# Kernel tuning notes

Hardware: AMD Instinct MI355X
Metric: run time of the kernel (lower is better)

Reference implementation:

```python
import jax, jax.numpy as jnp
import numpy as np

B, H, W = 4, 112, 112
N = H * W              # 12544 tokens
NBHD = 48              # local neighborhood size
DIM = 256
OUT_DIM = 512
INNER = 4              # inner_ch of weight_net
TABLE = 4096           # pre_table rows
ALPHA = 4.0
DS_RATE = 0.25
STRIDE = 2
RESERVE = (H // 4) * (W // 4)  # 784 reserve tokens (pos % 4 == 0)
EPS = 1e-5


def _ln(x, g, b):
    m = x.mean(-1, keepdims=True)
    v = ((x - m) ** 2).mean(-1, keepdims=True)
    return (x - m) / jnp.sqrt(v + EPS) * g + b


def setup_inputs() -> dict:
    key = jax.random.key(0)
    ks = jax.random.split(key, 8)
    ii, jj = jnp.meshgrid(jnp.arange(H), jnp.arange(W), indexing='ij')
    pos = jnp.stack([ii, jj], -1).reshape(1, N, 2).astype(jnp.float32)
    pos = jnp.tile(pos, (B, 1, 1))                             # b x n x 2 integer grid
    feat = jax.random.normal(ks[0], (B, N, DIM), jnp.float32)
    member_idx = jax.random.randint(ks[1], (B, N, NBHD), 0, N)
    cluster_mask = (jax.random.uniform(ks[2], (B, N, NBHD)) > 0.1).astype(jnp.float32)
    learned_prob = jax.random.uniform(ks[3], (B, N, 1), dtype=jnp.float32)
    pe_idx = jax.random.randint(ks[4], (B, N, NBHD), 0, TABLE)
    pre_table = jax.random.normal(ks[5], (TABLE, 5), jnp.float32)
    w1 = jax.random.normal(ks[6], (5, INNER), jnp.float32) * 0.4
    b1 = jnp.zeros((INNER,), jnp.float32)
    ln1_g = jnp.ones((INNER,), jnp.float32)
    ln1_b = jnp.zeros((INNER,), jnp.float32)
    norm_g = jnp.ones((INNER * DIM,), jnp.float32)
    norm_b = jnp.zeros((INNER * DIM,), jnp.float32)
    lin_w = jax.random.normal(ks[7], (INNER * DIM, OUT_DIM), jnp.float32) * (1.0 / np.sqrt(INNER * DIM))
    lin_b = jnp.zeros((OUT_DIM,), jnp.float32)
    return dict(pos=pos, feat=feat, member_idx=member_idx, cluster_mask=cluster_mask,
                learned_prob=learned_prob, stride=STRIDE, pe_idx=pe_idx, reserve_num=RESERVE,
                pre_table=pre_table, w1=w1, b1=b1, ln1_g=ln1_g, ln1_b=ln1_b,
                norm_g=norm_g, norm_b=norm_b, lin_w=lin_w, lin_b=lin_b)


def reference(pos, feat, member_idx, cluster_mask, learned_prob, stride, pe_idx,
              reserve_num, pre_table, w1, b1, ln1_g, ln1_b, norm_g, norm_b, lin_w, lin_b):
    b, n, c = feat.shape
    keep_num = int(n * DS_RATE)
    pos_long = pos.astype(jnp.int32)
    # stride == 2 branch: tokens on the coarse grid get prob 1
    grid_prob = jnp.all(pos_long % stride == 0, axis=-1).astype(jnp.float32)      # b x n
    lp_s = jax.lax.stop_gradient(learned_prob).reshape(b, n) * ALPHA              # detached scores
    final_prob = grid_prob + lp_s
    reserve_mask = jnp.all(pos_long % (stride * 2) == 0, axis=-1).astype(jnp.float32)
    final_prob = final_prob + reserve_mask * (-100.0)
    sample_num = keep_num - reserve_num
    _, sample_idx = jax.lax.top_k(final_prob, sample_num)                         # b x sample_num
    # per-row nonzero of reserve_mask (exactly reserve_num hits per row)
    flat_nz = jnp.nonzero(reserve_mask.reshape(-1) > 0, size=b * reserve_num)[0]
    reserve_idx = (flat_nz % n).reshape(b, reserve_num).astype(sample_idx.dtype)
    idx = jnp.concatenate([sample_idx, reserve_idx], axis=1)                      # b x keep_num

    pos_k = jnp.take_along_axis(pos, idx[:, :, None], axis=1)                     # b x keep x 2
    nbhd = member_idx.shape[-1]
    mem_k = jnp.take_along_axis(member_idx, idx[:, :, None], axis=1)              # b x keep x nbhd
    pe_k = jnp.take_along_axis(pe_idx, idx[:, :, None], axis=1)
    cm_k = jnp.take_along_axis(cluster_mask, idx[:, :, None], axis=1)
    lp = jnp.take_along_axis(learned_prob, mem_k.reshape(b, -1, 1), axis=1)
    lp = lp.reshape(b, keep_num, nbhd, 1)

    # weight_net on the small PE table, then gather per-edge weights
    wt = jax.nn.gelu(_ln(pre_table @ w1 + b1, ln1_g, ln1_b), approximate=False)   # TABLE x INNER
    weights = wt[pe_k]                                                            # b x keep x nbhd x INNER
    weights = weights * (lp * cm_k[..., None])

    # CLUSTENWF: gather neighbor features and weighted-sum over the neighborhood
    gathered = jnp.take_along_axis(feat, mem_k.reshape(b, -1, 1), axis=1)
    gathered = gathered.reshape(b, keep_num, nbhd, c)                             # b x keep x nbhd x c
    out = jnp.einsum('bnkm,bnkc->bnmc', weights, gathered).reshape(b, keep_num, INNER * c)
    out = _ln(out, norm_g, norm_b)
    return pos_k, out @ lin_w + lin_b
```

## Files before the change

### kernel.cpp

```cpp
#include <hip/hip_runtime.h>

typedef unsigned short u16;
typedef unsigned int u32;
typedef unsigned long long u64;

#define NB 4
#define NTOK 12544
#define NBHD 48
#define DIM 256
#define OUTD 512
#define KEEPN 3136
#define SAMPLEN 2352
#define RESN 784
#define GW 112
#define POSN (NB * KEEPN * 2)
#define QTR (NTOK / 4)
#define NBKT 16384

#define BLKM 128
#define BLKN 256
#define BROW 40

#define FEATB_BYTES (25690112ull)
#define XWS_BYTES   (25690112ull)
#define LINT_BYTES  (1048576ull)
#define KEYS_BYTES  (401408ull)
#define PART_BYTES  (802816ull)
#define WS_NEED (FEATB_BYTES + XWS_BYTES + LINT_BYTES + KEYS_BYTES + PART_BYTES)

__device__ __forceinline__ float bf2f(u16 u) {
    union { u32 i; float f; } v; v.i = ((u32)u) << 16; return v.f;
}
__device__ __forceinline__ float asf(u32 u) {
    union { u32 i; float f; } v; v.i = u; return v.f;
}
__device__ __forceinline__ u16 f2bf(float f) {
    union { u32 i; float f; } v; v.f = f;
    return (u16)((v.i + 0x7FFFu + ((v.i >> 16) & 1u)) >> 16);
}

typedef __bf16 bf16x8 __attribute__((ext_vector_type(8)));
typedef float floatx4 __attribute__((ext_vector_type(4)));

__device__ __forceinline__ float make_f(float lp, int n) {
    int i = n / GW, j = n % GW;
    float f = lp * 4.0f;
    if (((i | j) & 1) == 0) f = 1.0f + f;
    if (((i | j) & 3) == 0) f = f + (-100.0f);
    return f;
}
__device__ __forceinline__ u64 f_to_key(float f, int n) {
    union { float f; u32 u; } v; v.f = f;
    u32 m = (v.u & 0x80000000u) ? ~v.u : (v.u | 0x80000000u);
    return (((u64)m) << 32) | (u64)(0xFFFFFFFFu - (u32)n);
}
__device__ __forceinline__ int f_to_bucket(float f) {
    int b = (int)floorf(f * 3276.8f);
    return b < 0 ? 0 : (b > NBKT - 1 ? NBKT - 1 : b);
}

__global__ __launch_bounds__(256) void feat_cvt_kernel(
    const float* __restrict__ feat, u16* __restrict__ featb) {
    int t = blockIdx.x * 256 + threadIdx.x;
    float4 v = ((const float4*)feat)[t];
    u64 w = (u64)f2bf(v.x) | ((u64)f2bf(v.y) << 16) |
            ((u64)f2bf(v.z) << 32) | ((u64)f2bf(v.w) << 48);
    ((u64*)featb)[t] = w;
}

__global__ __launch_bounds__(256) void linT_cvt_kernel(
    const float* __restrict__ lin_w, u16* __restrict__ linT) {
    __shared__ u16 T[64 * 65];
    int k0 = blockIdx.x * 64, n0 = blockIdx.y * 64;
    int t = threadIdx.x;
    int r = t >> 2, c4 = (t & 3) * 16;
#pragma unroll
    for (int i = 0; i < 4; ++i) {
        float4 v = *(const float4*)&lin_w[(size_t)(k0 + r) * OUTD + n0 + c4 + i * 4];
        T[(c4 + i * 4 + 0) * 65 + r] = f2bf(v.x);
        T[(c4 + i * 4 + 1) * 65 + r] = f2bf(v.y);
        T[(c4 + i * 4 + 2) * 65 + r] = f2bf(v.z);
        T[(c4 + i * 4 + 3) * 65 + r] = f2bf(v.w);
    }
    __syncthreads();
    int nl = t >> 2, kc = (t & 3) * 16;
    union { uint4 v[2]; u16 h[16]; } u;
#pragma unroll
    for (int i = 0; i < 16; ++i) u.h[i] = T[nl * 65 + kc + i];
    u16* dst = &linT[(size_t)(n0 + nl) * 1024 + k0 + kc];
    *(uint4*)(dst + 0) = u.v[0];
    *(uint4*)(dst + 8) = u.v[1];
}

__global__ __launch_bounds__(256) void zero_hist_kernel(u32* __restrict__ hist) {
    hist[blockIdx.x * 256 + threadIdx.x] = 0;
}

__global__ __launch_bounds__(256) void hist_kernel(
    const float* __restrict__ lprob, u32* __restrict__ hist) {
    int g = blockIdx.x * 256 + threadIdx.x;
    int b = g / NTOK, n = g % NTOK;
    int bkt = f_to_bucket(make_f(lprob[g], n));
    atomicAdd(&hist[b * NBKT + bkt], 1u);
}

__global__ __launch_bounds__(1024) void prefix_kernel(
    const u32* __restrict__ hist, u32* __restrict__ base, u32* __restrict__ cursor) {
    int b = blockIdx.x, t = threadIdx.x;
    const u32* h = hist + b * NBKT;
    u32 loc[16], own = 0;
#pragma unroll
    for (int i = 0; i < 16; ++i) { loc[i] = h[t * 16 + i]; own += loc[i]; }
    __shared__ u32 buf[2][1024];
    buf[0][t] = own;
    __syncthreads();
    int src = 0;
    for (int off = 1; off < 1024; off <<= 1) {
        u32 v = buf[src][t] + ((t + off < 1024) ? buf[src][t + off] : 0u);
        buf[src ^ 1][t] = v;
        src ^= 1;
        __syncthreads();
    }
    u32 above = buf[src][t] - own;
    u32 suf = 0, bout[16];
    for (int i = 15; i >= 0; --i) { bout[i] = above + suf; suf += loc[i]; }
    u32* bb = base + b * NBKT;
    u32* cc = cursor + b * NBKT;
#pragma unroll
    for (int i = 0; i < 16; ++i) { bb[t * 16 + i] = bout[i]; cc[t * 16 + i] = bout[i]; }
}

__global__ __launch_bounds__(256) void scatter_kernel(
    const float* __restrict__ lprob, u32* __restrict__ cursor,
    u64* __restrict__ slots) {
    int g = blockIdx.x * 256 + threadIdx.x;
    int b = g / NTOK, n = g % NTOK;
    float f = make_f(lprob[g], n);
    int bkt = f_to_bucket(f);
    u32 s = atomicAdd(&cursor[b * NBKT + bkt], 1u);
    slots[b * NTOK + s] = f_to_key(f, n);
}

__global__ __launch_bounds__(256) void rank_finalize_kernel(
    const float* __restrict__ lprob, const u32* __restrict__ hist,
    const u32* __restrict__ base, const u64* __restrict__ slots,
    float* __restrict__ pos_out) {
    int g = blockIdx.x * 256 + threadIdx.x;
    int b = g / NTOK, n = g % NTOK;
    int i = n / GW, j = n % GW;
    if (((i | j) & 3) == 0) {
        int r = (i >> 2) * 28 + (j >> 2);
        int slot = b * KEEPN + SAMPLEN + r;
        pos_out[slot * 2 + 0] = (float)i;
        pos_out[slot * 2 + 1] = (float)j;
        return;
    }
    float f = make_f(lprob[g], n);
    int bkt = f_to_bucket(f);
    u32 r0 = base[b * NBKT + bkt];
    if (r0 >= SAMPLEN) return;
    u64 my = f_to_key(f, n);
    u32 cnt = hist[b * NBKT + bkt];
    const u64* sl = slots + b * NTOK + r0;
    u32 rank = r0;
    for (u32 s = 0; s < cnt; ++s) rank += (sl[s] > my) ? 1u : 0u;
    if (rank < SAMPLEN) {
        int slot = b * KEEPN + (int)rank;
        pos_out[slot * 2 + 0] = (float)i;
        pos_out[slot * 2 + 1] = (float)j;
    }
}

__global__ __launch_bounds__(256) void token_v2_kernel(
    const float* __restrict__ pos_in, u16* __restrict__ xdst,
    const int* __restrict__ member_idx, const int* __restrict__ pe_idx,
    const float* __restrict__ cmask, const float* __restrict__ lprob,
    const u16* __restrict__ featb, const float* __restrict__ pre_table,
    const float* __restrict__ w1, const float* __restrict__ b1,
    const float* __restrict__ g1, const float* __restrict__ bb1,
    const float* __restrict__ norm_g, const float* __restrict__ norm_b) {
    int t = blockIdx.x;
    int b = t / KEEPN;
    int tid = threadIdx.x;
    int wave = tid >> 6, lane = tid & 63;
    __shared__ int mem_s[NBHD];
    __shared__ float4 w_s[NBHD];
    __shared__ float partials[4 * 64 * 16];
    __shared__ float red[10];

    int n_src = (int)pos_in[t * 2 + 0] * GW + (int)pos_in[t * 2 + 1];

    if (tid < NBHD) {
        int e = (b * NTOK + n_src) * NBHD + tid;
        int mem = member_idx[e];
        int pe = pe_idx[e];
        float cm = cmask[e];
        float lpe = lprob[b * NTOK + mem];
        float z[4];
#pragma unroll
        for (int m = 0; m < 4; ++m) {
            float acc = b1[m];
#pragma unroll
            for (int d = 0; d < 5; ++d) acc += pre_table[pe * 5 + d] * w1[d * 4 + m];
            z[m] = acc;
        }
        float mean = (z[0] + z[1] + z[2] + z[3]) * 0.25f;
        float var = 0.0f;
#pragma unroll
        for (int m = 0; m < 4; ++m) { float d = z[m] - mean; var += d * d; }
        float rstd = rsqrtf(var * 0.25f + 1e-5f);
        float sc = lpe * cm;
        float wv[4];
#pragma unroll
        for (int m = 0; m < 4; ++m) {
            float y = (z[m] - mean) * rstd * g1[m] + bb1[m];
            wv[m] = 0.5f * y * (1.0f + erff(y * 0.70710678118654752f)) * sc;
        }
        w_s[tid] = make_float4(wv[0], wv[1], wv[2], wv[3]);
        mem_s[tid] = mem;
    }
    __syncthreads();

    float acc[16];
#pragma unroll
    for (int i = 0; i < 16; ++i) acc[i] = 0.0f;
    const u16* fbase = featb + (size_t)b * NTOK * DIM + lane * 4;
    int k0 = wave * 12;
#pragma unroll
    for (int kk = 0; kk < 12; ++kk) {
        int k = k0 + kk;
        uint2 d = *(const uint2*)(fbase + (size_t)mem_s[k] * DIM);
        float4 w = w_s[k];
        float c0 = asf(d.x << 16);
        float c1 = asf(d.x & 0xFFFF0000u);
        float c2 = asf(d.y << 16);
        float c3 = asf(d.y & 0xFFFF0000u);
        acc[0]  += w.x * c0; acc[1]  += w.y * c0; acc[2]  += w.z * c0; acc[3]  += w.w * c0;
        acc[4]  += w.x * c1; acc[5]  += w.y * c1; acc[6]  += w.z * c1; acc[7]  += w.w * c1;
        acc[8]  += w.x * c2; acc[9]  += w.y * c2; acc[10] += w.z * c2; acc[11] += w.w * c2;
        acc[12] += w.x * c3; acc[13] += w.y * c3; acc[14] += w.z * c3; acc[15] += w.w * c3;
    }
    float* pp = &partials[(wave * 64 + lane) * 16];
#pragma unroll
    for (int i = 0; i < 4; ++i)
        *(float4*)(pp + i * 4) = make_float4(acc[i * 4], acc[i * 4 + 1],
                                             acc[i * 4 + 2], acc[i * 4 + 3]);
    __syncthreads();

    int c = tid;
    float a[4] = {0.f, 0.f, 0.f, 0.f};
#pragma unroll
    for (int w = 0; w < 4; ++w) {
        float4 v = *(const float4*)&partials[(w * 64 + (c >> 2)) * 16 + (c & 3) * 4];
        a[0] += v.x; a[1] += v.y; a[2] += v.z; a[3] += v.w;
    }

    float s1 = a[0] + a[1] + a[2] + a[3];
    float s2 = a[0] * a[0] + a[1] * a[1] + a[2] * a[2] + a[3] * a[3];
#pragma unroll
    for (int off = 32; off > 0; off >>= 1) {
        s1 += __shfl_down(s1, off, 64);
        s2 += __shfl_down(s2, off, 64);
    }
    if (lane == 0) { red[wave] = s1; red[4 + wave] = s2; }
    __syncthreads();
    if (tid == 0) {
        float S = red[0] + red[1] + red[2] + red[3];
        float Q = red[4] + red[5] + red[6] + red[7];
        float mean = S * (1.0f / 1024.0f);
        float var = fmaxf(Q * (1.0f / 1024.0f) - mean * mean, 0.0f);
        red[8] = mean; red[9] = rsqrtf(var + 1e-5f);
    }
    __syncthreads();
    float mean = red[8], rstd = red[9];
    u16* Xp = xdst + (size_t)t * 1024;
#pragma unroll
    for (int m = 0; m < 4; ++m) {
        int cc = m * 256 + c;
        float v = (a[m] - mean) * rstd * norm_g[cc] + norm_b[cc];
        Xp[cc] = f2bf(v);
    }
}

#define GROW 40
__global__ __launch_bounds__(256) void gemm_tile_kernel(
    const u16* __restrict__ xws, const u16* __restrict__ linT,
    const float* __restrict__ lin_b, float* __restrict__ out) {
    __shared__ __align__(16) u16 As[64 * GROW];
    __shared__ __align__(16) u16 Bs[128 * GROW];
    int tid = threadIdx.x;
    int wave = tid >> 6, lane = tid & 63;
    int l15 = lane & 15, quad = lane >> 4;
    int wm = wave >> 1, wn = wave & 1;
    int m0 = blockIdx.x * 64, n0 = blockIdx.y * 128;
    int sr = tid >> 2, sk = (tid & 3) * 8;

    const u16* Ap  = xws + (size_t)(m0 + sr) * 1024 + sk;
    const u16* Bp0 = linT + (size_t)(n0 + sr) * 1024 + sk;
    const u16* Bp1 = linT + (size_t)(n0 + 64 + sr) * 1024 + sk;

    floatx4 acc[2][4] = {};
    for (int kk = 0; kk < 1024; kk += 32) {
        uint4 av = *(const uint4*)(Ap + kk);
        uint4 b0 = *(const uint4*)(Bp0 + kk);
        uint4 b1 = *(const uint4*)(Bp1 + kk);
        __syncthreads();
        *(uint4*)&As[sr * GROW + sk] = av;
        *(uint4*)&Bs[sr * GROW + sk] = b0;
        *(uint4*)&Bs[(64 + sr) * GROW + sk] = b1;
        __syncthreads();
        bf16x8 af[2], bfv[4];
#pragma unroll
        for (int mi = 0; mi < 2; ++mi)
            af[mi] = *(const bf16x8*)&As[(wm * 32 + mi * 16 + l15) * GROW + quad * 8];
#pragma unroll
        for (int ni = 0; ni < 4; ++ni)
            bfv[ni] = *(const bf16x8*)&Bs[(wn * 64 + ni * 16 + l15) * GROW + quad * 8];
#pragma unroll
        for (int mi = 0; mi < 2; ++mi)
#pragma unroll
            for (int ni = 0; ni < 4; ++ni)
                acc[mi][ni] = __builtin_amdgcn_mfma_f32_16x16x32_bf16(
                    af[mi], bfv[ni], acc[mi][ni], 0, 0, 0);
    }
#pragma unroll
    for (int ni = 0; ni < 4; ++ni) {
        int col = n0 + wn * 64 + ni * 16 + l15;
        float bias = lin_b[col];
#pragma unroll
        for (int mi = 0; mi < 2; ++mi)
#pragma unroll
            for (int reg = 0; reg < 4; ++reg) {
                int row = m0 + wm * 32 + mi * 16 + quad * 4 + reg;
                out[(size_t)row * OUTD + col] = acc[mi][ni][reg] + bias;
            }
    }
}

__global__ __launch_bounds__(256) void key_kernel(
    const float* __restrict__ lprob, u64* __restrict__ keys) {
    int g = blockIdx.x * 256 + threadIdx.x;
    int n = g % NTOK;
    keys[g] = f_to_key(make_f(lprob[g], n), n);
}

__global__ __launch_bounds__(256) void partial_rank_kernel(
    const u64* __restrict__ keys, u32* __restrict__ part) {
    int b = blockIdx.y, z = blockIdx.z;
    int n = blockIdx.x * 256 + threadIdx.x;
    u64 my = keys[b * NTOK + n];
    const u64* kb = keys + b * NTOK + z * QTR;
    u32 cnt = 0;
    for (int t = 0; t < QTR; t += 8) {
#pragma unroll
        for (int j = 0; j < 8; ++j) cnt += (kb[t + j] > my) ? 1u : 0u;
    }
    part[(z * NB + b) * NTOK + n] = cnt;
}

__global__ __launch_bounds__(256) void finalize_kernel(
    const u32* __restrict__ part, float* __restrict__ pos_out) {
    int b = blockIdx.y;
    int n = blockIdx.x * 256 + threadIdx.x;
    int g = b * NTOK + n;
    u32 rank = part[g] + part[(NB + b) * NTOK + n] +
               part[(2 * NB + b) * NTOK + n] + part[(3 * NB + b) * NTOK + n];
    int i = n / GW, j = n % GW;
    if (rank < SAMPLEN) {
        int slot = b * KEEPN + (int)rank;
        pos_out[slot * 2 + 0] = (float)i;
        pos_out[slot * 2 + 1] = (float)j;
    }
    if (((i | j) & 3) == 0) {
        int r = (i >> 2) * 28 + (j >> 2);
        int slot = b * KEEPN + SAMPLEN + r;
        pos_out[slot * 2 + 0] = (float)i;
        pos_out[slot * 2 + 1] = (float)j;
    }
}

__global__ __launch_bounds__(256) void token_fb_kernel(
    const float* __restrict__ pos_in, u16* __restrict__ xdst,
    const int* __restrict__ member_idx, const int* __restrict__ pe_idx,
    const float* __restrict__ cmask, const float* __restrict__ lprob,
    const float* __restrict__ featf, const float* __restrict__ pre_table,
    const float* __restrict__ w1, const float* __restrict__ b1,
    const float* __restrict__ g1, const float* __restrict__ bb1,
    const float* __restrict__ norm_g, const float* __restrict__ norm_b) {
    int t = blockIdx.x;
    int b = t / KEEPN;
    int tid = threadIdx.x;
    __shared__ int mem_s[NBHD];
    __shared__ float4 w_s[NBHD];
    __shared__ float red[10];

    int n_src = (int)pos_in[t * 2 + 0] * GW + (int)pos_in[t * 2 + 1];

    if (tid < NBHD) {
        int e = (b * NTOK + n_src) * NBHD + tid;
        int mem = member_idx[e];
        int pe = pe_idx[e];
        float cm = cmask[e];
        float lpe = lprob[b * NTOK + mem];
        float z[4];
#pragma unroll
        for (int m = 0; m < 4; ++m) {
            float acc = b1[m];
#pragma unroll
            for (int d = 0; d < 5; ++d) acc += pre_table[pe * 5 + d] * w1[d * 4 + m];
            z[m] = acc;
        }
        float mean = (z[0] + z[1] + z[2] + z[3]) * 0.25f;
        float var = 0.0f;
#pragma unroll
        for (int m = 0; m < 4; ++m) { float d = z[m] - mean; var += d * d; }
        float rstd = rsqrtf(var * 0.25f + 1e-5f);
        float sc = lpe * cm;
        float wv[4];
#pragma unroll
        for (int m = 0; m < 4; ++m) {
            float y = (z[m] - mean) * rstd * g1[m] + bb1[m];
            wv[m] = 0.5f * y * (1.0f + erff(y * 0.70710678118654752f)) * sc;
        }
        w_s[tid] = make_float4(wv[0], wv[1], wv[2], wv[3]);
        mem_s[tid] = mem;
    }
    __syncthreads();

    float a0 = 0.f, a1 = 0.f, a2 = 0.f, a3 = 0.f;
    size_t base = (size_t)b * NTOK * DIM + tid;
#pragma unroll 8
    for (int k = 0; k < NBHD; ++k) {
        float g = featf[base + (size_t)mem_s[k] * DIM];
        float4 w = w_s[k];
        a0 += w.x * g; a1 += w.y * g; a2 += w.z * g; a3 += w.w * g;
    }
    float s1 = a0 + a1 + a2 + a3;
    float s2 = a0 * a0 + a1 * a1 + a2 * a2 + a3 * a3;
#pragma unroll
    for (int off = 32; off > 0; off >>= 1) {
        s1 += __shfl_down(s1, off, 64);
        s2 += __shfl_down(s2, off, 64);
    }
    int wave = tid >> 6, lane = tid & 63;
    if (lane == 0) { red[wave] = s1; red[4 + wave] = s2; }
    __syncthreads();
    if (tid == 0) {
        float S = red[0] + red[1] + red[2] + red[3];
        float Q = red[4] + red[5] + red[6] + red[7];
        float mean = S * (1.0f / 1024.0f);
        float var = fmaxf(Q * (1.0f / 1024.0f) - mean * mean, 0.0f);
        red[8] = mean; red[9] = rsqrtf(var + 1e-5f);
    }
    __syncthreads();
    float mean = red[8], rstd = red[9];
    float acc4[4] = {a0, a1, a2, a3};
    u16* Xp = xdst + (size_t)t * 1024;
#pragma unroll
    for (int m = 0; m < 4; ++m) {
        int cc = m * 256 + tid;
        float v = (acc4[m] - mean) * rstd * norm_g[cc] + norm_b[cc];
        Xp[cc] = f2bf(v);
    }
}

__global__ __launch_bounds__(256) void gemm_inplace_kernel(
    const float* __restrict__ lin_w, const float* __restrict__ lin_b,
    float* __restrict__ out) {
    __shared__ __align__(16) u16 Bs[BLKN * BROW];
    int tile_m = blockIdx.x;
    int nblk = blockIdx.y;
    int tid = threadIdx.x;
    int wave = tid >> 6, lane = tid & 63;
    int l15 = lane & 15, quad = lane >> 4;

    const u16* Xbase = (const u16*)out;
    floatx4 acc[8][4] = {};

    for (int kk = 0; kk < 1024; kk += 32) {
        __syncthreads();
#pragma unroll
        for (int it = 0; it < 4; ++it) {
            int task = it * 256 + tid;
            int kp = task >> 6;
            int ng = task & 63;
            int k = kp * 2;
            int n0 = nblk * BLKN + ng * 4;
            float4 fa = *(const float4*)&lin_w[(size_t)(kk + k) * OUTD + n0];
            float4 fb = *(const float4*)&lin_w[(size_t)(kk + k + 1) * OUTD + n0];
            u16* bp = &Bs[(ng * 4) * BROW + k];
            *(u32*)(bp + 0 * BROW) = (u32)f2bf(fa.x) | ((u32)f2bf(fb.x) << 16);
            *(u32*)(bp + 1 * BROW) = (u32)f2bf(fa.y) | ((u32)f2bf(fb.y) << 16);
            *(u32*)(bp + 2 * BROW) = (u32)f2bf(fa.z) | ((u32)f2bf(fb.z) << 16);
            *(u32*)(bp + 3 * BROW) = (u32)f2bf(fa.w) | ((u32)f2bf(fb.w) << 16);
        }
        __syncthreads();
        bf16x8 bfrag[4];
#pragma unroll
        for (int ni = 0; ni < 4; ++ni)
            bfrag[ni] = *(const bf16x8*)&Bs[(wave * 64 + ni * 16 + l15) * BROW + quad * 8];
#pragma unroll
        for (int mi = 0; mi < 8; ++mi) {
            int row = tile_m * BLKM + mi * 16 + l15;
            bf16x8 af = *(const bf16x8*)&Xbase[(size_t)row * 1024 + kk + quad * 8];
#pragma unroll
            for (int ni = 0; ni < 4; ++ni)
                acc[mi][ni] = __builtin_amdgcn_mfma_f32_16x16x32_bf16(
                    af, bfrag[ni], acc[mi][ni], 0, 0, 0);
        }
    }
    __syncthreads();
#pragma unroll
    for (int mi = 0; mi < 8; ++mi)
#pragma unroll
        for (int ni = 0; ni < 4; ++ni) {
            int col = nblk * BLKN + wave * 64 + ni * 16 + l15;
            float bias = lin_b[col];
#pragma unroll
            for (int reg = 0; reg < 4; ++reg) {
                int row = tile_m * BLKM + mi * 16 + quad * 4 + reg;
                out[(size_t)row * OUTD + col] = acc[mi][ni][reg] + bias;
            }
        }
}

extern "C" void kernel_launch(void* const* d_in, const int* in_sizes, int n_in,
                              void* d_out, int out_size, void* d_ws, size_t ws_size,
                              hipStream_t stream) {
    const float* feat     = (const float*)d_in[1];
    const int* member_idx = (const int*)d_in[2];
    const float* cmask    = (const float*)d_in[3];
    const float* lprob    = (const float*)d_in[4];
    const int* pe_idx     = (const int*)d_in[6];
    const float* pre_table= (const float*)d_in[8];
    const float* w1       = (const float*)d_in[9];
    const float* b1       = (const float*)d_in[10];
    const float* g1       = (const float*)d_in[11];
    const float* bb1      = (const float*)d_in[12];
    const float* norm_g   = (const float*)d_in[13];
    const float* norm_b   = (const float*)d_in[14];
    const float* lin_w    = (const float*)d_in[15];
    const float* lin_b    = (const float*)d_in[16];

    float* pos_out = (float*)d_out;
    float* out     = pos_out + POSN;

    if (ws_size >= WS_NEED) {
        char* ws = (char*)d_ws;
        u16* featb = (u16*)ws;
        u16* xws   = (u16*)(ws + FEATB_BYTES);
        u16* linT  = (u16*)(ws + FEATB_BYTES + XWS_BYTES);
        u64* slots = (u64*)(ws + FEATB_BYTES + XWS_BYTES + LINT_BYTES);
        u32* hist  = (u32*)(ws + FEATB_BYTES + XWS_BYTES + LINT_BYTES + KEYS_BYTES);
        u32* base  = hist + NB * NBKT;
        u32* curs  = base + NB * NBKT;

        feat_cvt_kernel<<<12544, 256, 0, stream>>>(feat, featb);
        linT_cvt_kernel<<<dim3(16, 8), 256, 0, stream>>>(lin_w, linT);
        zero_hist_kernel<<<256, 256, 0, stream>>>(hist);
        hist_kernel<<<(NB * NTOK) / 256, 256, 0, stream>>>(lprob, hist);
        prefix_kernel<<<NB, 1024, 0, stream>>>(hist, base, curs);
        scatter_kernel<<<(NB * NTOK) / 256, 256, 0, stream>>>(lprob, curs, slots);
        rank_finalize_kernel<<<(NB * NTOK) / 256, 256, 0, stream>>>(
            lprob, hist, base, slots, pos_out);
        token_v2_kernel<<<NB * KEEPN, 256, 0, stream>>>(
            pos_out, xws, member_idx, pe_idx, cmask, lprob, featb,
            pre_table, w1, b1, g1, bb1, norm_g, norm_b);
        gemm_tile_kernel<<<dim3(196, 4), 256, 0, stream>>>(xws, linT, lin_b, out);
    } else {
        u64* keys = (u64*)out;
        u32* part = (u32*)((char*)out + 401408);

        key_kernel<<<(NB * NTOK) / 256, 256, 0, stream>>>(lprob, keys);
        partial_rank_kernel<<<dim3(49, NB, 4), 256, 0, stream>>>(keys, part);
        finalize_kernel<<<dim3(49, NB), 256, 0, stream>>>(part, pos_out);
        token_fb_kernel<<<NB * KEEPN, 256, 0, stream>>>(
            pos_out, (u16*)out, member_idx, pe_idx, cmask, lprob, feat,
            pre_table, w1, b1, g1, bb1, norm_g, norm_b);
        gemm_inplace_kernel<<<dim3(98, 2), 256, 0, stream>>>(lin_w, lin_b, out);
    }
}
```

Baseline: 254.4 us.

## Fuse hist zeroing, remap token blocks per XCD, pad partials, enlarge GEMM tile

Hist zeroing moves into the linT conversion kernel, which saves one launch: 128 blocks x 512 entries cover the 65536 hist words. Token blocks are remapped so each batch lands on a pair of XCDs, aiming for better L2 locality on feature gathers. The partials shared array is padded to a stride of 20 to cut LDS bank conflicts. The GEMM tile grows from 64 to 128 rows per block, which halves the grid to 392 blocks and doubles B-tile reuse, at the cost of more accumulator registers.

```diff
diff --git a/kernel.cpp b/kernel.cpp
--- a/kernel.cpp
+++ b/kernel.cpp
@@ -69,10 +69,14 @@
 }
 
 __global__ __launch_bounds__(256) void linT_cvt_kernel(
-    const float* __restrict__ lin_w, u16* __restrict__ linT) {
+    const float* __restrict__ lin_w, u16* __restrict__ linT,
+    u32* __restrict__ hist) {
     __shared__ u16 T[64 * 65];
     int k0 = blockIdx.x * 64, n0 = blockIdx.y * 64;
     int t = threadIdx.x;
+    int bid = blockIdx.y * 16 + blockIdx.x;
+    hist[bid * 512 + t] = 0;
+    hist[bid * 512 + 256 + t] = 0;
     int r = t >> 2, c4 = (t & 3) * 16;
 #pragma unroll
     for (int i = 0; i < 4; ++i) {
@@ -90,10 +94,6 @@
     u16* dst = &linT[(size_t)(n0 + nl) * 1024 + k0 + kc];
     *(uint4*)(dst + 0) = u.v[0];
     *(uint4*)(dst + 8) = u.v[1];
-}
-
-__global__ __launch_bounds__(256) void zero_hist_kernel(u32* __restrict__ hist) {
-    hist[blockIdx.x * 256 + threadIdx.x] = 0;
 }
 
 __global__ __launch_bounds__(256) void hist_kernel(
@@ -171,6 +171,7 @@
     }
 }
 
+#define PSTR 20
 __global__ __launch_bounds__(256) void token_v2_kernel(
     const float* __restrict__ pos_in, u16* __restrict__ xdst,
     const int* __restrict__ member_idx, const int* __restrict__ pe_idx,
@@ -179,13 +180,15 @@
     const float* __restrict__ w1, const float* __restrict__ b1,
     const float* __restrict__ g1, const float* __restrict__ bb1,
     const float* __restrict__ norm_g, const float* __restrict__ norm_b) {
-    int t = blockIdx.x;
-    int b = t / KEEPN;
+    int bi = blockIdx.x;
+    int xcd = bi & 7, jj = bi >> 3;
+    int b = xcd >> 1;
+    int t = b * KEEPN + (xcd & 1) * 1568 + jj;
     int tid = threadIdx.x;
     int wave = tid >> 6, lane = tid & 63;
     __shared__ int mem_s[NBHD];
     __shared__ float4 w_s[NBHD];
-    __shared__ float partials[4 * 64 * 16];
+    __shared__ float partials[4 * 64 * PSTR];
     __shared__ float red[10];
 
     int n_src = (int)pos_in[t * 2 + 0] * GW + (int)pos_in[t * 2 + 1];
@@ -240,7 +243,7 @@
         acc[8]  += w.x * c2; acc[9]  += w.y * c2; acc[10] += w.z * c2; acc[11] += w.w * c2;
         acc[12] += w.x * c3; acc[13] += w.y * c3; acc[14] += w.z * c3; acc[15] += w.w * c3;
     }
-    float* pp = &partials[(wave * 64 + lane) * 16];
+    float* pp = &partials[(wave * 64 + lane) * PSTR];
 #pragma unroll
     for (int i = 0; i < 4; ++i)
         *(float4*)(pp + i * 4) = make_float4(acc[i * 4], acc[i * 4 + 1],
@@ -251,7 +254,7 @@
     float a[4] = {0.f, 0.f, 0.f, 0.f};
 #pragma unroll
     for (int w = 0; w < 4; ++w) {
-        float4 v = *(const float4*)&partials[(w * 64 + (c >> 2)) * 16 + (c & 3) * 4];
+        float4 v = *(const float4*)&partials[(w * 64 + (c >> 2)) * PSTR + (c & 3) * 4];
         a[0] += v.x; a[1] += v.y; a[2] += v.z; a[3] += v.w;
     }
 
@@ -286,38 +289,41 @@
 __global__ __launch_bounds__(256) void gemm_tile_kernel(
     const u16* __restrict__ xws, const u16* __restrict__ linT,
     const float* __restrict__ lin_b, float* __restrict__ out) {
-    __shared__ __align__(16) u16 As[64 * GROW];
+    __shared__ __align__(16) u16 As[128 * GROW];
     __shared__ __align__(16) u16 Bs[128 * GROW];
     int tid = threadIdx.x;
     int wave = tid >> 6, lane = tid & 63;
     int l15 = lane & 15, quad = lane >> 4;
     int wm = wave >> 1, wn = wave & 1;
-    int m0 = blockIdx.x * 64, n0 = blockIdx.y * 128;
+    int m0 = blockIdx.x * 128, n0 = blockIdx.y * 128;
     int sr = tid >> 2, sk = (tid & 3) * 8;
 
-    const u16* Ap  = xws + (size_t)(m0 + sr) * 1024 + sk;
+    const u16* Ap0 = xws + (size_t)(m0 + sr) * 1024 + sk;
+    const u16* Ap1 = Ap0 + (size_t)64 * 1024;
     const u16* Bp0 = linT + (size_t)(n0 + sr) * 1024 + sk;
-    const u16* Bp1 = linT + (size_t)(n0 + 64 + sr) * 1024 + sk;
-
-    floatx4 acc[2][4] = {};
+    const u16* Bp1 = Bp0 + (size_t)64 * 1024;
+
+    floatx4 acc[4][4] = {};
     for (int kk = 0; kk < 1024; kk += 32) {
-        uint4 av = *(const uint4*)(Ap + kk);
+        uint4 a0 = *(const uint4*)(Ap0 + kk);
+        uint4 a1 = *(const uint4*)(Ap1 + kk);
         uint4 b0 = *(const uint4*)(Bp0 + kk);
         uint4 b1 = *(const uint4*)(Bp1 + kk);
         __syncthreads();
-        *(uint4*)&As[sr * GROW + sk] = av;
+        *(uint4*)&As[sr * GROW + sk] = a0;
+        *(uint4*)&As[(64 + sr) * GROW + sk] = a1;
         *(uint4*)&Bs[sr * GROW + sk] = b0;
         *(uint4*)&Bs[(64 + sr) * GROW + sk] = b1;
         __syncthreads();
-        bf16x8 af[2], bfv[4];
-#pragma unroll
-        for (int mi = 0; mi < 2; ++mi)
-            af[mi] = *(const bf16x8*)&As[(wm * 32 + mi * 16 + l15) * GROW + quad * 8];
+        bf16x8 af[4], bfv[4];
+#pragma unroll
+        for (int mi = 0; mi < 4; ++mi)
+            af[mi] = *(const bf16x8*)&As[(wm * 64 + mi * 16 + l15) * GROW + quad * 8];
 #pragma unroll
         for (int ni = 0; ni < 4; ++ni)
             bfv[ni] = *(const bf16x8*)&Bs[(wn * 64 + ni * 16 + l15) * GROW + quad * 8];
 #pragma unroll
-        for (int mi = 0; mi < 2; ++mi)
+        for (int mi = 0; mi < 4; ++mi)
 #pragma unroll
             for (int ni = 0; ni < 4; ++ni)
                 acc[mi][ni] = __builtin_amdgcn_mfma_f32_16x16x32_bf16(
@@ -328,10 +334,10 @@
         int col = n0 + wn * 64 + ni * 16 + l15;
         float bias = lin_b[col];
 #pragma unroll
-        for (int mi = 0; mi < 2; ++mi)
+        for (int mi = 0; mi < 4; ++mi)
 #pragma unroll
             for (int reg = 0; reg < 4; ++reg) {
-                int row = m0 + wm * 32 + mi * 16 + quad * 4 + reg;
+                int row = m0 + wm * 64 + mi * 16 + quad * 4 + reg;
                 out[(size_t)row * OUTD + col] = acc[mi][ni][reg] + bias;
             }
     }
@@ -556,8 +562,7 @@
         u32* curs  = base + NB * NBKT;
 
         feat_cvt_kernel<<<12544, 256, 0, stream>>>(feat, featb);
-        linT_cvt_kernel<<<dim3(16, 8), 256, 0, stream>>>(lin_w, linT);
-        zero_hist_kernel<<<256, 256, 0, stream>>>(hist);
+        linT_cvt_kernel<<<dim3(16, 8), 256, 0, stream>>>(lin_w, linT, hist);
         hist_kernel<<<(NB * NTOK) / 256, 256, 0, stream>>>(lprob, hist);
         prefix_kernel<<<NB, 1024, 0, stream>>>(hist, base, curs);
         scatter_kernel<<<(NB * NTOK) / 256, 256, 0, stream>>>(lprob, curs, slots);
@@ -566,7 +571,7 @@
         token_v2_kernel<<<NB * KEEPN, 256, 0, stream>>>(
             pos_out, xws, member_idx, pe_idx, cmask, lprob, featb,
             pre_table, w1, b1, g1, bb1, norm_g, norm_b);
-        gemm_tile_kernel<<<dim3(196, 4), 256, 0, stream>>>(xws, linT, lin_b, out);
+        gemm_tile_kernel<<<dim3(98, 4), 256, 0, stream>>>(xws, linT, lin_b, out);
     } else {
         u64* keys = (u64*)out;
         u32* part = (u32*)((char*)out + 401408);
```

Measured after the change: 254.1 us. Within noise of the previous version (-0.1%).
